# Kernel optimization log

Measured on AMD Instinct MI355X. Metric: run time of the kernel, lower is better.

## Reference

```python
import math
import jax, jax.numpy as jnp
import numpy as np

D_MODEL = 1024
NHEAD = 16
HEAD_DIM = D_MODEL // NHEAD
BATCH = 2
SEQ = 2048


def setup_inputs() -> dict:
    key = jax.random.key(0)
    ks = jax.random.split(key, 8)
    data = jax.random.normal(ks[0], (BATCH, SEQ, D_MODEL), dtype=jnp.float32)
    temporal = jax.random.uniform(ks[1], (BATCH, SEQ), dtype=jnp.float32)
    mask = jnp.zeros((SEQ, SEQ), dtype=jnp.float32)
    s = 1.0 / math.sqrt(D_MODEL)
    Wq = jax.random.normal(ks[2], (D_MODEL, D_MODEL), dtype=jnp.float32) * s
    Wk = jax.random.normal(ks[3], (D_MODEL, D_MODEL), dtype=jnp.float32) * s
    Wv = jax.random.normal(ks[4], (D_MODEL, D_MODEL), dtype=jnp.float32) * s
    bq = jax.random.normal(ks[5], (D_MODEL,), dtype=jnp.float32) * 0.02
    bk = jax.random.normal(ks[6], (D_MODEL,), dtype=jnp.float32) * 0.02
    bv = jax.random.normal(ks[7], (D_MODEL,), dtype=jnp.float32) * 0.02
    return {"data": data, "temporal": temporal, "mask": mask,
            "Wq": Wq, "bq": bq, "Wk": Wk, "bk": bk, "Wv": Wv, "bv": bv}


def _rotate_half_pairs(x):
    # x: [..., s] with s even; pairs (x0,x1) -> (-x1, x0) interleaved
    x2 = x.reshape(x.shape[:-1] + (-1, 2))  # [..., s//2, 2]
    rot = jnp.stack([-x2[..., 1], x2[..., 0]], axis=-1)
    return rot.reshape(x.shape)


def reference(data, temporal, mask, Wq, bq, Wk, bk, Wv, bv):
    B, L, D = data.shape
    H, S = NHEAD, HEAD_DIM
    scale = math.sqrt(S)

    query = (data @ Wq + bq).reshape(B, L, H, S)
    key_ = (data @ Wk + bk).reshape(B, L, H, S)
    value = (data @ Wv + bv).reshape(B, L, H, S)

    # freq = 10000^(-arange(0, S, 2)/S), repeat_interleave(2) -> [S]
    freq = jnp.power(10000.0, -jnp.arange(0, S, 2, dtype=jnp.float32) / S)
    freq = jnp.repeat(freq, 2)
    freqs = temporal[:, :, None] * freq[None, None, :]  # [B, L, S]
    cosine = jnp.cos(freqs)[:, :, None, :]  # [B, L, 1, S]
    sine = jnp.sin(freqs)[:, :, None, :]

    rq = query * cosine + _rotate_half_pairs(query) * sine
    rk = key_ * cosine + _rotate_half_pairs(key_) * sine

    logits = jnp.einsum('bqhs,bkhs->bhqk', rq, rk) / scale
    logits = logits + mask  # mask: [L, L], broadcasts over b,h
    weights = jax.nn.softmax(logits, axis=-1)
    context = jnp.einsum('bhqk,bkhs->bqhs', weights, value)
    return context.reshape(B, L, D)
```

## Files before the change

kernel.cpp:

```cpp
#include <hip/hip_runtime.h>
#include <hip/hip_bf16.h>

#define D_MODEL 1024
#define NHEAD   16
#define HEAD_DIM 64
#define BATCH   2
#define SEQ     2048
#define NTOK    (BATCH*SEQ)

#define FREQ_LOG2 0.20762050593046015f

typedef short  bfrag __attribute__((ext_vector_type(8)));
typedef float  ffrag __attribute__((ext_vector_type(4)));

__device__ inline ushort f2bf(float x) {
    __hip_bfloat16 h = __float2bfloat16(x);
    return __builtin_bit_cast(ushort, h);
}
__device__ inline float bf2f(ushort u) {
    return __builtin_bit_cast(float, (uint)u << 16);
}
__device__ inline void split_bf(float x, ushort& hi, ushort& lo) {
    __hip_bfloat16 h = __float2bfloat16(x);
    hi = __builtin_bit_cast(ushort, h);
    lo = f2bf(x - __bfloat162float(h));
}

__device__ inline void gload16(const ushort* g, ushort* l) {
    __builtin_amdgcn_global_load_lds(
        (const __attribute__((address_space(1))) void*)g,
        (__attribute__((address_space(3))) void*)l, 16, 0, 0);
}

__device__ inline void barrier_lds_only() {
    asm volatile("s_waitcnt lgkmcnt(0)\n\ts_barrier" ::: "memory");
}

__device__ inline void barrier_vm4() {
    asm volatile("s_waitcnt vmcnt(4) lgkmcnt(0)\n\ts_barrier" ::: "memory");
}

__global__ __launch_bounds__(256)
void prep(const float* __restrict__ data, ushort* __restrict__ Ahi,
          ushort* __restrict__ Alo,
          const float* __restrict__ mask, ushort* __restrict__ Mbf,
          int* __restrict__ MZnz,
          const float* __restrict__ Wq, const float* __restrict__ Wk,
          const float* __restrict__ Wv, ushort* __restrict__ WThi,
          const float* __restrict__ temporal, float* __restrict__ cst)
{
    __shared__ float T[64][65];
    __shared__ int bnz;
    const int bid = blockIdx.x, t = threadIdx.x;

    if (bid < 4096) {
        const int i4 = (bid * 256 + t) * 4;
        const float4 v = *(const float4*)(data + i4);
        ushort4 h, l;
        split_bf(v.x, h.x, l.x); split_bf(v.y, h.y, l.y);
        split_bf(v.z, h.z, l.z); split_bf(v.w, h.w, l.w);
        *(ushort4*)(Ahi + i4) = h;
        *(ushort4*)(Alo + i4) = l;
        return;
    }
    if (bid < 8192) {
        const int mi = bid - 4096;
        const int i4 = (mi * 256 + t) * 4;
        const float4 v = *(const float4*)(mask + i4);
        ushort4 h;
        h.x = f2bf(v.x); h.y = f2bf(v.y); h.z = f2bf(v.z); h.w = f2bf(v.w);
        *(ushort4*)(Mbf + i4) = h;
        const int nz = (v.x != 0.f) || (v.y != 0.f) || (v.z != 0.f) || (v.w != 0.f);
        if (t == 0) bnz = 0;
        __syncthreads();
        if (nz) atomicOr(&bnz, 1);
        __syncthreads();
        if (t == 0) MZnz[mi] = bnz;
        return;
    }
    if (bid < 8960) {
        const int id  = bid - 8192;
        const int z   = id >> 8;
        const int rem = id & 255;
        const int k0  = (rem & 15) * 64, n0 = (rem >> 4) * 64;
        const float* W = (z == 0) ? Wq : (z == 1) ? Wk : Wv;
        ushort* thi = WThi + (size_t)z * D_MODEL * D_MODEL;

        #pragma unroll
        for (int i = 0; i < 4; i++) {
            const int f = i * 256 + t, r = f >> 4, c = (f & 15) * 4;
            const float4 v = *(const float4*)(W + (size_t)(k0 + r) * D_MODEL + n0 + c);
            T[r][c] = v.x; T[r][c + 1] = v.y; T[r][c + 2] = v.z; T[r][c + 3] = v.w;
        }
        __syncthreads();
        #pragma unroll
        for (int i = 0; i < 4; i++) {
            const int f = i * 256 + t, nr = f >> 4, kc = (f & 15) * 4;
            ushort4 h;
            h.x = f2bf(T[kc + 0][nr]);
            h.y = f2bf(T[kc + 1][nr]);
            h.z = f2bf(T[kc + 2][nr]);
            h.w = f2bf(T[kc + 3][nr]);
            const size_t o = (size_t)(n0 + nr) * D_MODEL + k0 + kc;
            *(ushort4*)(thi + o) = h;
        }
        return;
    }
    const int id3 = bid - 8960;
    const int m   = id3 * 8 + (t >> 5);
    const int j   = t & 31;
    const float tv = temporal[m];
    const float fr = exp2f(-(float)(2 * j) * FREQ_LOG2);
    float s, c;
    __sincosf(tv * fr, &s, &c);
    *(float2*)(cst + (size_t)m * 64 + 2 * j) = make_float2(c, s);
}

#define BK 32

union GemmSM {
    ushort st[2][2][128 * BK];
    float  c[64 * 132];
};

__global__ __launch_bounds__(256, 4)
void gemm_qkv(const ushort* __restrict__ Ahi, const ushort* __restrict__ Alo,
              const ushort* __restrict__ WThi,
              const float* __restrict__ bq, const float* __restrict__ bk,
              const float* __restrict__ bv, const float* __restrict__ cst,
              const int* __restrict__ MZnz, int* __restrict__ Flag,
              ushort* __restrict__ Qhi, ushort* __restrict__ Qlo,
              ushort* __restrict__ Khi,
              ushort* __restrict__ VT)
{
    __shared__ GemmSM sm;
    __shared__ int flg;
    const int bidl = blockIdx.x;
    const int xcd  = bidl & 7, kk = bidl >> 3;
    const int m0   = (xcd * 4 + (kk & 3)) * 128;
    const int nz   = kk >> 2;
    const int n0   = (nz & 7) * 128;
    const int z    = nz >> 3;

    const int t = threadIdx.x;

    if (bidl == 0) {
        if (t == 0) flg = 0;
        __syncthreads();
        int acc = 0;
        const int4* z4 = (const int4*)MZnz;
        #pragma unroll
        for (int i = 0; i < 4; i++) {
            const int4 v = z4[t * 4 + i];
            acc |= v.x | v.y | v.z | v.w;
        }
        if (acc) atomicOr(&flg, 1);
        __syncthreads();
        if (t == 0) Flag[0] = flg;
    }

    const float* bias = (z == 0) ? bq : (z == 1) ? bk : bv;
    const ushort* Bh = WThi + (size_t)z * D_MODEL * D_MODEL;

    const int w = t >> 6, lane = t & 63;
    const int lane15 = lane & 15, quad8 = (lane >> 4) * 8, quad = lane >> 4;
    const int wm = (w >> 1) * 64, wn = (w & 1) * 64;

    ffrag acc[4][4];
    #pragma unroll
    for (int i = 0; i < 4; i++)
        #pragma unroll
        for (int j = 0; j < 4; j++) acc[i][j] = (ffrag){0.f, 0.f, 0.f, 0.f};

    const int wr = w * 32;
    const int lr = lane >> 2;
    const int lc = (((lane & 3) ^ ((lane >> 3) & 3))) * 8;

    auto stage = [&](int bsel, int k0) {
        #pragma unroll
        for (int ch = 0; ch < 2; ch++) {
            const int rb = wr + ch * 16;
            const ushort* ga = Ahi + (size_t)(m0 + rb + lr) * D_MODEL + k0 + lc;
            const ushort* gb = Bh  + (size_t)(n0 + rb + lr) * D_MODEL + k0 + lc;
            gload16(ga, &sm.st[bsel][0][rb * BK]);
            gload16(gb, &sm.st[bsel][1][rb * BK]);
        }
    };

    const size_t arow[1] = {0};
    bfrag alp0, alp1, alp2, alp3;
    {
        const size_t r0 = (size_t)(m0 + wm +  0 + lane15) * D_MODEL + quad8;
        const size_t r1_ = (size_t)(m0 + wm + 16 + lane15) * D_MODEL + quad8;
        const size_t r2 = (size_t)(m0 + wm + 32 + lane15) * D_MODEL + quad8;
        const size_t r3 = (size_t)(m0 + wm + 48 + lane15) * D_MODEL + quad8;
        alp0 = *(const bfrag*)(Alo + r0);
        alp1 = *(const bfrag*)(Alo + r1_);
        alp2 = *(const bfrag*)(Alo + r2);
        alp3 = *(const bfrag*)(Alo + r3);
    }

    stage(0, 0);
    __syncthreads();

    const int rdsw = (quad ^ ((lane15 >> 1) & 3)) * 8;

    int buf = 0;
    for (int k0 = 0; k0 < D_MODEL; k0 += BK) {
        if (k0 + BK < D_MODEL) stage(buf ^ 1, k0 + BK);

        bfrag al0 = alp0, al1 = alp1, al2 = alp2, al3 = alp3;
        if (k0 + BK < D_MODEL) {
            const int kn = k0 + BK;
            alp0 = *(const bfrag*)(Alo + (size_t)(m0 + wm +  0 + lane15) * D_MODEL + kn + quad8);
            alp1 = *(const bfrag*)(Alo + (size_t)(m0 + wm + 16 + lane15) * D_MODEL + kn + quad8);
            alp2 = *(const bfrag*)(Alo + (size_t)(m0 + wm + 32 + lane15) * D_MODEL + kn + quad8);
            alp3 = *(const bfrag*)(Alo + (size_t)(m0 + wm + 48 + lane15) * D_MODEL + kn + quad8);
        }

        bfrag ah[4];
        #pragma unroll
        for (int mt = 0; mt < 4; mt++)
            ah[mt] = *(const bfrag*)&sm.st[buf][0][(wm + mt * 16 + lane15) * BK + rdsw];

        #pragma unroll
        for (int nt = 0; nt < 4; nt++) {
            const bfrag bh = *(const bfrag*)&sm.st[buf][1][(wn + nt * 16 + lane15) * BK + rdsw];
            {
                ffrag a = acc[0][nt];
                a = __builtin_amdgcn_mfma_f32_16x16x32_bf16(ah[0], bh, a, 0, 0, 0);
                a = __builtin_amdgcn_mfma_f32_16x16x32_bf16(al0,   bh, a, 0, 0, 0);
                acc[0][nt] = a;
            }
            {
                ffrag a = acc[1][nt];
                a = __builtin_amdgcn_mfma_f32_16x16x32_bf16(ah[1], bh, a, 0, 0, 0);
                a = __builtin_amdgcn_mfma_f32_16x16x32_bf16(al1,   bh, a, 0, 0, 0);
                acc[1][nt] = a;
            }
            {
                ffrag a = acc[2][nt];
                a = __builtin_amdgcn_mfma_f32_16x16x32_bf16(ah[2], bh, a, 0, 0, 0);
                a = __builtin_amdgcn_mfma_f32_16x16x32_bf16(al2,   bh, a, 0, 0, 0);
                acc[2][nt] = a;
            }
            {
                ffrag a = acc[3][nt];
                a = __builtin_amdgcn_mfma_f32_16x16x32_bf16(ah[3], bh, a, 0, 0, 0);
                a = __builtin_amdgcn_mfma_f32_16x16x32_bf16(al3,   bh, a, 0, 0, 0);
                acc[3][nt] = a;
            }
        }
        barrier_vm4();
        buf ^= 1;
    }

    float bn[4];
    #pragma unroll
    for (int nt = 0; nt < 4; nt++) bn[nt] = bias[n0 + wn + nt * 16 + lane15];

    const int CST = (z == 2) ? 129 : 132;

    #pragma unroll
    for (int p = 0; p < 2; p++) {
        if (p) __syncthreads();
        if ((w >> 1) == p) {
            #pragma unroll
            for (int mt = 0; mt < 4; mt++)
                #pragma unroll
                for (int nt = 0; nt < 4; nt++)
                    #pragma unroll
                    for (int rr = 0; rr < 4; rr++)
                        sm.c[(mt * 16 + quad * 4 + rr) * CST + wn + nt * 16 + lane15] =
                            acc[mt][nt][rr] + bn[nt];
        }
        __syncthreads();

        if (z < 2) {
            ushort* ohi = (z == 0) ? Qhi : Khi;
            const float sc = (z == 0) ? 0.125f : 1.0f;
            #pragma unroll
            for (int i = 0; i < 8; i++) {
                const int f = i * 256 + t, r = f >> 5, c4 = (f & 31) * 4;
                float4 v = *(float4*)&sm.c[r * 132 + c4];
                const int m = m0 + p * 64 + r;
                const float4 cs4 = *(const float4*)(cst + (size_t)m * 64 + (c4 & 63));
                const float c0 = cs4.x, s0 = cs4.y, c1v = cs4.z, s1 = cs4.w;
                const float y0 = (v.x * c0 - v.y * s0) * sc;
                const float y1 = (v.y * c0 + v.x * s0) * sc;
                const float y2 = (v.z * c1v - v.w * s1) * sc;
                const float y3 = (v.w * c1v + v.z * s1) * sc;
                ushort4 h, l;
                split_bf(y0, h.x, l.x); split_bf(y1, h.y, l.y);
                split_bf(y2, h.z, l.z); split_bf(y3, h.w, l.w);
                const size_t o = (size_t)m * D_MODEL + n0 + c4;
                *(ushort4*)(ohi + o) = h;
                if (z == 0) *(ushort4*)(Qlo + o) = l;
            }
        } else {
            const int bb = m0 >> 11;
            #pragma unroll
            for (int i = 0; i < 4; i++) {
                const int cid = i * 256 + t, col = cid >> 3, tg = (cid & 7) * 8;
                ushort u8[8];
                #pragma unroll
                for (int j = 0; j < 8; j++) u8[j] = f2bf(sm.c[(tg + j) * 129 + col]);
                const int ncol = n0 + col, hh = ncol >> 6, d = ncol & 63;
                const size_t dst = ((size_t)(bb * NHEAD + hh) * HEAD_DIM + d) * SEQ +
                                   (m0 & (SEQ - 1)) + p * 64 + tg;
                *(int4*)(VT + dst) = *(int4*)u8;
            }
        }
    }
}

__global__ __launch_bounds__(256, 2)
void attn_mfma(const ushort* __restrict__ Qhi, const ushort* __restrict__ Qlo,
               const ushort* __restrict__ Khi,
               const ushort* __restrict__ VT,  const ushort* __restrict__ maskbf,
               const int* __restrict__ Flag,
               float* __restrict__ out)
{
    __shared__ ushort lsK[2][64 * 64], lsV[2][64 * 64], lsP[128 * 64];

    const int bid  = blockIdx.x;
    const int bh   = (bid & 7) * 4 + (bid >> 7);
    const int qb   = (bid >> 3) & 15;
    const int b    = bh >> 4, h = bh & 15;
    const int q0   = qb * 128;

    const int t = threadIdx.x, w = t >> 6, lane = t & 63;
    const int lane15 = lane & 15, quad = lane >> 4;
    const size_t tok0 = (size_t)b * SEQ;

    const int mz = Flag[0];

    bfrag qh[2][2], ql[2][2];
    #pragma unroll
    for (int su = 0; su < 2; su++) {
        const size_t qrow = (tok0 + q0 + w * 32 + su * 16 + lane15) * D_MODEL +
                            h * HEAD_DIM;
        #pragma unroll
        for (int ks = 0; ks < 2; ks++) {
            qh[su][ks] = *(const bfrag*)(Qhi + qrow + ks * 32 + quad * 8);
            ql[su][ks] = *(const bfrag*)(Qlo + qrow + ks * 32 + quad * 8);
        }
    }

    ffrag of[2][4];
    float l_i[2][4];
    #pragma unroll
    for (int su = 0; su < 2; su++)
        #pragma unroll
        for (int nt = 0; nt < 4; nt++) {
            of[su][nt] = (ffrag){0.f, 0.f, 0.f, 0.f};
            l_i[su][nt] = 0.f;
        }

    const int r1 = t >> 3,  c1 = (t & 7) * 8;
    const int sw = ((t & 7) ^ (r1 & 7)) * 8;
    const ushort* Kh0 = Khi + tok0 * D_MODEL + h * HEAD_DIM;
    const ushort* Vt0 = VT + (size_t)(b * NHEAD + h) * HEAD_DIM * SEQ;

    int4 pk0 = *(const int4*)(Kh0 + (size_t)r1 * D_MODEL + c1);
    int4 pk1 = *(const int4*)(Kh0 + (size_t)(32 + r1) * D_MODEL + c1);
    int4 pv0 = *(const int4*)(Vt0 + (size_t)r1 * SEQ + c1);
    int4 pv1 = *(const int4*)(Vt0 + (size_t)(32 + r1) * SEQ + c1);

    *(int4*)&lsK[0][r1 * 64 + sw]        = pk0;
    *(int4*)&lsK[0][(32 + r1) * 64 + sw] = pk1;
    *(int4*)&lsV[0][r1 * 64 + sw]        = pv0;
    *(int4*)&lsV[0][(32 + r1) * 64 + sw] = pv1;

    pk0 = *(const int4*)(Kh0 + (size_t)(64 + r1) * D_MODEL + c1);
    pk1 = *(const int4*)(Kh0 + (size_t)(96 + r1) * D_MODEL + c1);
    pv0 = *(const int4*)(Vt0 + (size_t)r1 * SEQ + 64 + c1);
    pv1 = *(const int4*)(Vt0 + (size_t)(32 + r1) * SEQ + 64 + c1);
    barrier_lds_only();

    const ushort* mrow0 = maskbf + (size_t)(q0 + w * 32 + quad * 4) * SEQ;
    const ushort* mrow1 = maskbf + (size_t)(q0 + w * 32 + 16 + quad * 4) * SEQ;

    const int krd  = lane15 & 7;
    const int keyr = (((lane15 >> 2) & 3) << 1) | (lane15 & 1);

    int cur = 0;
    for (int kt = 0; kt < SEQ; kt += 64) {
        if (kt + 64 < SEQ) {
            *(int4*)&lsK[cur ^ 1][r1 * 64 + sw]        = pk0;
            *(int4*)&lsK[cur ^ 1][(32 + r1) * 64 + sw] = pk1;
            *(int4*)&lsV[cur ^ 1][r1 * 64 + sw]        = pv0;
            *(int4*)&lsV[cur ^ 1][(32 + r1) * 64 + sw] = pv1;
        }

        float mv0[4][4], mv1[4][4];
        if (mz) {
            #pragma unroll
            for (int nt = 0; nt < 4; nt++)
                #pragma unroll
                for (int rr = 0; rr < 4; rr++) {
                    mv0[nt][rr] = bf2f(mrow0[(size_t)rr * SEQ + kt + nt * 16 + lane15]);
                    mv1[nt][rr] = bf2f(mrow1[(size_t)rr * SEQ + kt + nt * 16 + lane15]);
                }
        }

        const int ktn = (kt + 128 < SEQ) ? kt + 128 : 0;
        pk0 = *(const int4*)(Kh0 + (size_t)(ktn + r1) * D_MODEL + c1);
        pk1 = *(const int4*)(Kh0 + (size_t)(ktn + 32 + r1) * D_MODEL + c1);
        pv0 = *(const int4*)(Vt0 + (size_t)r1 * SEQ + ktn + c1);
        pv1 = *(const int4*)(Vt0 + (size_t)(32 + r1) * SEQ + ktn + c1);

        ffrag s0[4], s1[4];
        __builtin_amdgcn_s_setprio(1);
        #pragma unroll
        for (int nt = 0; nt < 4; nt++) {
            const bfrag kf0 = *(const bfrag*)&lsK[cur][(nt * 16 + lane15) * 64 +
                                                       ((0 + quad) ^ krd) * 8];
            const bfrag kf1 = *(const bfrag*)&lsK[cur][(nt * 16 + lane15) * 64 +
                                                       ((4 + quad) ^ krd) * 8];
            ffrag a0 = (ffrag){0.f, 0.f, 0.f, 0.f};
            ffrag a1 = (ffrag){0.f, 0.f, 0.f, 0.f};
            a0 = __builtin_amdgcn_mfma_f32_16x16x32_bf16(qh[0][0], kf0, a0, 0, 0, 0);
            a0 = __builtin_amdgcn_mfma_f32_16x16x32_bf16(ql[0][0], kf0, a0, 0, 0, 0);
            a0 = __builtin_amdgcn_mfma_f32_16x16x32_bf16(qh[0][1], kf1, a0, 0, 0, 0);
            a0 = __builtin_amdgcn_mfma_f32_16x16x32_bf16(ql[0][1], kf1, a0, 0, 0, 0);
            a1 = __builtin_amdgcn_mfma_f32_16x16x32_bf16(qh[1][0], kf0, a1, 0, 0, 0);
            a1 = __builtin_amdgcn_mfma_f32_16x16x32_bf16(ql[1][0], kf0, a1, 0, 0, 0);
            a1 = __builtin_amdgcn_mfma_f32_16x16x32_bf16(qh[1][1], kf1, a1, 0, 0, 0);
            a1 = __builtin_amdgcn_mfma_f32_16x16x32_bf16(ql[1][1], kf1, a1, 0, 0, 0);
            s0[nt] = a0;
            s1[nt] = a1;
        }
        __builtin_amdgcn_s_setprio(0);

        #pragma unroll
        for (int nt = 0; nt < 4; nt++)
            #pragma unroll
            for (int rr = 0; rr < 4; rr++) {
                const int pchk = (2 * nt + (lane15 >> 3)) ^ ((quad << 1) | (rr & 1));
                float x0 = s0[nt][rr];
                float x1 = s1[nt][rr];
                if (mz) { x0 += mv0[nt][rr]; x1 += mv1[nt][rr]; }
                const float e0 = __expf(x0);
                l_i[0][rr] += e0;
                lsP[(w * 32 + quad * 4 + rr) * 64 + pchk * 8 + (lane15 & 7)] = f2bf(e0);
                const float e1 = __expf(x1);
                l_i[1][rr] += e1;
                lsP[(w * 32 + 16 + quad * 4 + rr) * 64 + pchk * 8 + (lane15 & 7)] = f2bf(e1);
            }

        __builtin_amdgcn_s_setprio(1);
        #pragma unroll
        for (int ks = 0; ks < 2; ks++) {
            const bfrag pf0 = *(const bfrag*)&lsP[(w * 32 + lane15) * 64 +
                                                  ((ks * 4 + quad) ^ keyr) * 8];
            const bfrag pf1 = *(const bfrag*)&lsP[(w * 32 + 16 + lane15) * 64 +
                                                  ((ks * 4 + quad) ^ keyr) * 8];
            #pragma unroll
            for (int nt = 0; nt < 4; nt++) {
                const bfrag vf = *(const bfrag*)&lsV[cur][(nt * 16 + lane15) * 64 +
                                                          ((ks * 4 + quad) ^ krd) * 8];
                of[0][nt] = __builtin_amdgcn_mfma_f32_16x16x32_bf16(pf0, vf, of[0][nt], 0, 0, 0);
                of[1][nt] = __builtin_amdgcn_mfma_f32_16x16x32_bf16(pf1, vf, of[1][nt], 0, 0, 0);
            }
        }
        __builtin_amdgcn_s_setprio(0);

        barrier_lds_only();
        cur ^= 1;
    }

    #pragma unroll
    for (int su = 0; su < 2; su++) {
        float inv[4];
        #pragma unroll
        for (int rr = 0; rr < 4; rr++) {
            float v = l_i[su][rr];
            #pragma unroll
            for (int off = 1; off < 16; off <<= 1) v += __shfl_xor(v, off);
            inv[rr] = 1.0f / v;
        }
        #pragma unroll
        for (int nt = 0; nt < 4; nt++)
            #pragma unroll
            for (int rr = 0; rr < 4; rr++)
                out[(tok0 + q0 + w * 32 + su * 16 + quad * 4 + rr) * D_MODEL +
                    h * HEAD_DIM + nt * 16 + lane15] = of[su][nt][rr] * inv[rr];
    }
}

extern "C" void kernel_launch(void* const* d_in, const int* in_sizes, int n_in,
                              void* d_out, int out_size, void* d_ws, size_t ws_size,
                              hipStream_t stream)
{
    const float* data     = (const float*)d_in[0];
    const float* temporal = (const float*)d_in[1];
    const float* mask     = (const float*)d_in[2];
    const float* Wq = (const float*)d_in[3];
    const float* bq = (const float*)d_in[4];
    const float* Wk = (const float*)d_in[5];
    const float* bk = (const float*)d_in[6];
    const float* Wv = (const float*)d_in[7];
    const float* bv = (const float*)d_in[8];
    float* out = (float*)d_out;

    char* ws = (char*)d_ws;
    const size_t MB = 1024 * 1024;
    ushort* Ahi  = (ushort*)(ws + 0 * MB);
    ushort* Alo  = (ushort*)(ws + 8 * MB);
    ushort* WThi = (ushort*)(ws + 16 * MB);
    int*    MZnz = (int*)   (ws + 22 * MB);
    int*    Flag = (int*)   (ws + 23 * MB);
    float*  cst  = (float*) (ws + 24 * MB);
    ushort* Qhi  = (ushort*)(ws + 28 * MB);
    ushort* Qlo  = (ushort*)(ws + 36 * MB);
    ushort* Khi  = (ushort*)(ws + 44 * MB);
    ushort* VT   = (ushort*)(ws + 60 * MB);
    ushort* Mbf  = (ushort*)(ws + 68 * MB);

    prep<<<dim3(9472), 256, 0, stream>>>(data, Ahi, Alo, mask, Mbf, MZnz,
                                         Wq, Wk, Wv, WThi, temporal, cst);
    gemm_qkv<<<dim3(768), 256, 0, stream>>>(
        Ahi, Alo, WThi, bq, bk, bv, cst, MZnz, Flag,
        Qhi, Qlo, Khi, VT);
    attn_mfma<<<dim3(BATCH * NHEAD * SEQ / 128), 256, 0, stream>>>(
        Qhi, Qlo, Khi, VT, Mbf, Flag, out);
}
```

Before: 249.4 us.

## Triple-buffer LDS staging in QKV GEMM with deeper async prefetch

The QKV projection GEMM moves from double to triple buffering of its LDS tiles. Two K-slices are prefetched before the loop, and each iteration issues the load for slice k+2, so global_load_lds has more time to land. The barrier now waits with vmcnt(8) rather than vmcnt(4), which keeps the newest iteration's loads in flight. The larger shared buffer lowers the launch-bounds occupancy hint from 4 to 3 blocks. The last two iterations also prefetch unused slices just past the K extent, which may read slightly beyond the end of the array.

```diff
diff --git a/kernel.cpp b/kernel.cpp
--- a/kernel.cpp
+++ b/kernel.cpp
@@ -38,6 +38,10 @@
 
 __device__ inline void barrier_vm4() {
     asm volatile("s_waitcnt vmcnt(4) lgkmcnt(0)\n\ts_barrier" ::: "memory");
+}
+
+__device__ inline void barrier_vm8() {
+    asm volatile("s_waitcnt vmcnt(8) lgkmcnt(0)\n\ts_barrier" ::: "memory");
 }
 
 __global__ __launch_bounds__(256)
@@ -119,11 +123,11 @@
 #define BK 32
 
 union GemmSM {
-    ushort st[2][2][128 * BK];
+    ushort st[3][2][128 * BK];
     float  c[64 * 132];
 };
 
-__global__ __launch_bounds__(256, 4)
+__global__ __launch_bounds__(256, 3)
 void gemm_qkv(const ushort* __restrict__ Ahi, const ushort* __restrict__ Alo,
               const ushort* __restrict__ WThi,
               const float* __restrict__ bq, const float* __restrict__ bk,
@@ -187,30 +191,28 @@
         }
     };
 
-    const size_t arow[1] = {0};
     bfrag alp0, alp1, alp2, alp3;
     {
-        const size_t r0 = (size_t)(m0 + wm +  0 + lane15) * D_MODEL + quad8;
-        const size_t r1_ = (size_t)(m0 + wm + 16 + lane15) * D_MODEL + quad8;
-        const size_t r2 = (size_t)(m0 + wm + 32 + lane15) * D_MODEL + quad8;
-        const size_t r3 = (size_t)(m0 + wm + 48 + lane15) * D_MODEL + quad8;
-        alp0 = *(const bfrag*)(Alo + r0);
-        alp1 = *(const bfrag*)(Alo + r1_);
-        alp2 = *(const bfrag*)(Alo + r2);
-        alp3 = *(const bfrag*)(Alo + r3);
+        alp0 = *(const bfrag*)(Alo + (size_t)(m0 + wm +  0 + lane15) * D_MODEL + quad8);
+        alp1 = *(const bfrag*)(Alo + (size_t)(m0 + wm + 16 + lane15) * D_MODEL + quad8);
+        alp2 = *(const bfrag*)(Alo + (size_t)(m0 + wm + 32 + lane15) * D_MODEL + quad8);
+        alp3 = *(const bfrag*)(Alo + (size_t)(m0 + wm + 48 + lane15) * D_MODEL + quad8);
     }
 
     stage(0, 0);
-    __syncthreads();
+    stage(1, BK);
+    barrier_vm4();
 
     const int rdsw = (quad ^ ((lane15 >> 1) & 3)) * 8;
 
-    int buf = 0;
-    for (int k0 = 0; k0 < D_MODEL; k0 += BK) {
-        if (k0 + BK < D_MODEL) stage(buf ^ 1, k0 + BK);
+    int cur = 0;
+    for (int i = 0; i < 32; i++) {
+        const int k0 = i * BK;
+        const int st2 = (cur >= 1) ? cur - 1 : 2;
+        stage(st2, k0 + 2 * BK);
 
         bfrag al0 = alp0, al1 = alp1, al2 = alp2, al3 = alp3;
-        if (k0 + BK < D_MODEL) {
+        {
             const int kn = k0 + BK;
             alp0 = *(const bfrag*)(Alo + (size_t)(m0 + wm +  0 + lane15) * D_MODEL + kn + quad8);
             alp1 = *(const bfrag*)(Alo + (size_t)(m0 + wm + 16 + lane15) * D_MODEL + kn + quad8);
@@ -221,11 +223,11 @@
         bfrag ah[4];
         #pragma unroll
         for (int mt = 0; mt < 4; mt++)
-            ah[mt] = *(const bfrag*)&sm.st[buf][0][(wm + mt * 16 + lane15) * BK + rdsw];
+            ah[mt] = *(const bfrag*)&sm.st[cur][0][(wm + mt * 16 + lane15) * BK + rdsw];
 
         #pragma unroll
         for (int nt = 0; nt < 4; nt++) {
-            const bfrag bh = *(const bfrag*)&sm.st[buf][1][(wn + nt * 16 + lane15) * BK + rdsw];
+            const bfrag bh = *(const bfrag*)&sm.st[cur][1][(wn + nt * 16 + lane15) * BK + rdsw];
             {
                 ffrag a = acc[0][nt];
                 a = __builtin_amdgcn_mfma_f32_16x16x32_bf16(ah[0], bh, a, 0, 0, 0);
@@ -251,8 +253,8 @@
                 acc[3][nt] = a;
             }
         }
-        barrier_vm4();
-        buf ^= 1;
+        barrier_vm8();
+        cur = (cur == 2) ? 0 : cur + 1;
     }
 
     float bn[4];
```

After: 239.7 us. 1.04x faster.
